# Kernel tuning notes

Measured on AMD Instinct MI355X. Metric: run time of the kernel, lower is better.

The kernel has to match this reference:

```python
import jax, jax.numpy as jnp
import numpy as np

V, B, S, DI, DH, DO = 32000, 32, 512, 256, 512, 128


def setup_inputs() -> dict:
    key = jax.random.key(0)
    ks = jax.random.split(key, 10)
    w = lambda k, shape: (jax.random.normal(k, shape, jnp.float32) * 0.02)
    z = lambda n: jnp.zeros((n,), jnp.float32)
    return {
        "tokens": jax.random.randint(ks[0], (B, S), 0, V, dtype=jnp.int32),
        "emb": w(ks[1], (V, DI)),
        "l0_Wz": w(ks[2], (DI + DH, DH)), "l0_bz": z(DH),
        "l0_Wr": w(ks[3], (DI + DH, DH)), "l0_br": z(DH),
        "l0_Wn": w(ks[4], (DI + DH, DH)), "l0_bn": z(DH),
        "l1_Wz": w(ks[5], (DH + DH, DH)), "l1_bz": z(DH),
        "l1_Wr": w(ks[6], (DH + DH, DH)), "l1_br": z(DH),
        "l1_Wn": w(ks[7], (DH + DH, DH)), "l1_bn": z(DH),
        "fc_W": w(ks[8], (DH, DO)), "fc_b": z(DO),
    }


def gru_layer(x_seq, Wz, bz, Wr, br, Wn, bn):
    # x_seq: [B, S, Din]; hidden dim inferred from Wz
    dh = Wz.shape[1]
    h0 = jnp.zeros((x_seq.shape[0], dh), x_seq.dtype)

    def step(H, x_t):
        comb = jnp.concatenate([x_t, H], axis=-1)          # [B, Din+DH]
        Z = jax.nn.sigmoid(comb @ Wz + bz)
        Rg = jax.nn.sigmoid(comb @ Wr + br)
        comb2 = jnp.concatenate([x_t, Rg * H], axis=-1)
        H_tilde = jnp.tanh(comb2 @ Wn + bn)
        Hn = (1.0 - Z) * H + Z * H_tilde
        return Hn, Hn

    _, ys = jax.lax.scan(step, h0, jnp.swapaxes(x_seq, 0, 1))  # [S, B, DH]
    return jnp.swapaxes(ys, 0, 1)                              # [B, S, DH]


def reference(tokens, emb,
              l0_Wz, l0_bz, l0_Wr, l0_br, l0_Wn, l0_bn,
              l1_Wz, l1_bz, l1_Wr, l1_br, l1_Wn, l1_bn,
              fc_W, fc_b):
    x = emb[tokens]                                            # [B, S, DI]
    x = gru_layer(x, l0_Wz, l0_bz, l0_Wr, l0_br, l0_Wn, l0_bn)
    x = gru_layer(x, l1_Wz, l1_bz, l1_Wr, l1_br, l1_Wn, l1_bn)
    logits = x @ fc_W + fc_b                                   # [B, S, DO]
    return jax.nn.log_softmax(logits, axis=-1)
```

## Files before the change

### kernel.cpp

```cpp
#include <hip/hip_runtime.h>
#include <hip/hip_bf16.h>
#include <cstdint>
#include <cstddef>


typedef short v8ss __attribute__((ext_vector_type(8)));
typedef float v4f  __attribute__((ext_vector_type(4)));
typedef unsigned short u16x8 __attribute__((ext_vector_type(8)));
typedef unsigned long long u64;

#define MFMA16(a, b, c) __builtin_amdgcn_mfma_f32_16x16x32_bf16((a), (b), (c), 0, 0, 0)

__device__ __forceinline__ unsigned short f2bf(float f) {
  union { float f; unsigned u; } v; v.f = f;
  unsigned r = v.u + 0x7fffu + ((v.u >> 16) & 1u);
  return (unsigned short)(r >> 16);
}
__device__ __forceinline__ unsigned short f2bfp(float f) {
  unsigned short h = f2bf(f);
  return (h == 0x8080u) ? (unsigned short)0x8081u : h;
}
__device__ __forceinline__ float bf2f(unsigned short h) {
  union { unsigned u; float f; } v; v.u = ((unsigned)h) << 16; return v.f;
}

#define S64   0x8080808080808080ull
#define INF64 0x7F807F807F807F80ull
#define POLL_LIM 16384

__device__ __forceinline__ u64 aload(const u64* p) {
  return __hip_atomic_load(p, __ATOMIC_RELAXED, __HIP_MEMORY_SCOPE_AGENT);
}
__device__ __forceinline__ void astore(u64* p, u64 v) {
  __hip_atomic_store(p, v, __ATOMIC_RELAXED, __HIP_MEMORY_SCOPE_AGENT);
}
__device__ __forceinline__ u64 spin8(const u64* p, int* dead) {
  u64 v = aload(p);
  if (v != S64) return v;
  int it = 0;
  for (;;) {
    __builtin_amdgcn_s_sleep(1);
    v = aload(p);
    if (v != S64) return v;
    if (*(volatile int*)dead) return v;
    if (++it > POLL_LIM) { *(volatile int*)dead = 1; return v; }
  }
}

#define BB   32
#define SS   512
#define DI   256
#define DH   512
#define DO   128
#define MROWS (BB * SS)
#define SLAB 16384

#define O_HX0   0
#define O_HX1   16809984
#define O_RHX0  33619968
#define O_RHX1  50397184
#define O_WT0X  67174400
#define O_WT0H  (O_WT0X + 1536*256*2)
#define O_WT1X  (O_WT0H + 16*96*512*2)
#define O_WT1H  (O_WT1X + 1536*512*2)
#define O_WTFC  (O_WT1H + 16*96*512*2)
#define O_XEMB  (O_WTFC + 128*512*2)

__global__ void prep_kernel(const float* __restrict__ l0Wz, const float* __restrict__ l0Wr,
                            const float* __restrict__ l0Wn,
                            const float* __restrict__ l1Wz, const float* __restrict__ l1Wr,
                            const float* __restrict__ l1Wn,
                            const float* __restrict__ fcW,
                            unsigned short* __restrict__ Wt0x, unsigned short* __restrict__ Wt0h,
                            unsigned short* __restrict__ Wt1x, unsigned short* __restrict__ Wt1h,
                            unsigned short* __restrict__ WtFC) {
  const int n0 = 1536 * 256;
  const int n1 = 16 * 96 * 512;
  const int n2 = 1536 * 512;
  const int n3 = 16 * 96 * 512;
  const int n4 = 128 * 512;
  const int total = n0 + n1 + n2 + n3 + n4;
  for (int i = blockIdx.x * 256 + threadIdx.x; i < total; i += gridDim.x * 256) {
    int j = i;
    if (j < n0) {
      int gcol = j / 256, k = j % 256, g = gcol >> 9, c = gcol & 511;
      const float* W = g == 0 ? l0Wz : (g == 1 ? l0Wr : l0Wn);
      Wt0x[j] = f2bf(W[k * 512 + c]); continue;
    }
    j -= n0;
    if (j < n1) {
      int r = j / (96 * 512), rem = j % (96 * 512), row = rem / 512, k = rem % 512;
      int g = row >> 5, c = r * 32 + (row & 31);
      const float* W = g == 0 ? l0Wz : (g == 1 ? l0Wr : l0Wn);
      Wt0h[j] = f2bf(W[(256 + k) * 512 + c]); continue;
    }
    j -= n1;
    if (j < n2) {
      int gcol = j / 512, k = j % 512, g = gcol >> 9, c = gcol & 511;
      const float* W = g == 0 ? l1Wz : (g == 1 ? l1Wr : l1Wn);
      Wt1x[j] = f2bf(W[k * 512 + c]); continue;
    }
    j -= n2;
    if (j < n3) {
      int r = j / (96 * 512), rem = j % (96 * 512), row = rem / 512, k = rem % 512;
      int g = row >> 5, c = r * 32 + (row & 31);
      const float* W = g == 0 ? l1Wz : (g == 1 ? l1Wr : l1Wn);
      Wt1h[j] = f2bf(W[(512 + k) * 512 + c]); continue;
    }
    j -= n3;
    { int c = j / 512, k = j % 512; WtFC[j] = f2bf(fcW[k * 128 + c]); }
  }
}

__global__ void embed_kernel(const int* __restrict__ tokens, const float* __restrict__ emb,
                             unsigned short* __restrict__ Xemb) {
  int r = blockIdx.x;
  int c = threadIdx.x;
  int t = r >> 5, b = r & 31;
  int tok = tokens[b * SS + t];
  Xemb[(size_t)r * DI + c] = f2bf(emb[(size_t)tok * DI + c]);
}

template <int LAYER>
__device__ __forceinline__ void gru_body(
    const int g, const int role, const int tid,
    const unsigned short* __restrict__ WtH,
    const unsigned short* __restrict__ Wx,
    const unsigned short* __restrict__ Xe,
    unsigned short* hx0,
    unsigned short* hx, unsigned short* rhx,
    const float* __restrict__ bz, const float* __restrict__ br,
    const float* __restrict__ bn,
    unsigned short* Wt, unsigned short* At, unsigned short* Rt, unsigned short* Xt,
    float* zbuf, float* hbuf, unsigned short* rstage, unsigned short* hstage,
    int* dead) {
  constexpr int K = LAYER ? 512 : 256;

  for (int ch = tid; ch < 96 * 64; ch += 256) {
    int row = ch >> 6, off = (ch & 63) * 8;
    *(u16x8*)&Wt[row * 520 + off] = *(const u16x8*)&WtH[((size_t)role * 96 + row) * 512 + off];
  }
  for (int i = tid * 8; i < 16 * 520; i += 256 * 8) {
    *(u16x8*)&At[i] = (u16x8)0;
    *(u16x8*)&Rt[i] = (u16x8)0;
    *(u16x8*)&Xt[i] = (u16x8)0;
  }
  if (tid < 128) { zbuf[tid] = 0.f; hbuf[tid] = 0.f; }
  __syncthreads();

  const int w = tid >> 6, l = tid & 63, cl = l & 15, kg = l >> 4;
  const int gate = w >> 1;
  const int lc16 = (w & 1) * 16;
  const int colA = role * 32 + lc16 + cl;
  const float biasA = (gate ? br : bz)[colA];
  const int lc16b = (w & 1) * 16;
  const int colB = role * 32 + lc16b + cl;
  const float biasB = (w < 2) ? bn[colB] : 0.f;

  const size_t gofs = (size_t)g * 2048;
  u64* atdst = (u64*)&At[(tid >> 6) * 520 + (tid & 63) * 8];
  u64* xtdst = (u64*)&Xt[(tid >> 6) * 520 + (tid & 63) * 8];
  const size_t pubofs = gofs + (size_t)(tid >> 3) * 512 + role * 32 + (tid & 7) * 4;
  const unsigned short* WxA = Wx + (size_t)(gate * 512 + colA) * K;
  const unsigned short* WxB = Wx + (size_t)(1024 + colB) * K;

  for (int t = 0; t < SS; ++t) {
    if (LAYER == 0) {
      if (tid < 128) {
        int j = tid >> 5, off = (tid & 31) * 8;
        *(u16x8*)&Xt[j * 520 + off] =
            *(const u16x8*)&Xe[((size_t)(t * 32) + 4 * g + j) * 256 + off];
      }
    } else {
      const u64* p = (const u64*)(hx0 + (size_t)(t + 1) * SLAB + gofs) + tid * 2;
      u64 lo = spin8(p, dead), hi = spin8(p + 1, dead);
      xtdst[0] = lo; xtdst[1] = hi;
    }
    {
      const u64* p = (const u64*)(hx + (size_t)t * SLAB + gofs) + tid * 2;
      u64 lo = spin8(p, dead), hi = spin8(p + 1, dead);
      atdst[0] = lo; atdst[1] = hi;
    }
    __syncthreads();
    if (*(volatile int*)dead) break;

    {
      v4f acc = {};
#pragma unroll
      for (int kc = 0; kc < K / 32; ++kc) {
        int ko = kc * 32 + kg * 8;
        v8ss a = *(const v8ss*)&Xt[cl * 520 + ko];
        v8ss b = *(const v8ss*)&WxA[ko];
        acc = MFMA16(a, b, acc);
      }
#pragma unroll
      for (int kc = 0; kc < 16; ++kc) {
        int ko = kc * 32 + kg * 8;
        v8ss a = *(const v8ss*)&At[cl * 520 + ko];
        v8ss b = *(const v8ss*)&Wt[(gate * 32 + lc16 + cl) * 520 + ko];
        acc = MFMA16(a, b, acc);
      }
      if (l < 16) {
        int lc = lc16 + cl;
#pragma unroll
        for (int j = 0; j < 4; ++j) {
          float pre = acc[j] + biasA;
          float gv = 1.f / (1.f + __expf(-pre));
          if (gate == 0) zbuf[j * 32 + lc] = gv;
          else           rstage[j * 32 + lc] = f2bfp(gv * hbuf[j * 32 + lc]);
        }
      }
    }
    __syncthreads();
    if (tid < 32)
      astore((u64*)(rhx + (size_t)t * SLAB + pubofs),
             *(const u64*)&rstage[(tid >> 3) * 32 + (tid & 7) * 4]);

    v4f accB = {};
    if (w >= 2) {
      int tt = tid & 127;
      int row = tt >> 5, c16 = (tt & 31) * 16;
      const u64* p = (const u64*)(rhx + (size_t)t * SLAB + gofs + (size_t)row * 512 + c16);
      u64* d = (u64*)&Rt[row * 520 + c16];
      d[0] = spin8(p, dead);     d[1] = spin8(p + 1, dead);
      d[2] = spin8(p + 2, dead); d[3] = spin8(p + 3, dead);
    } else {
#pragma unroll
      for (int kc = 0; kc < K / 32; ++kc) {
        int ko = kc * 32 + kg * 8;
        v8ss a = *(const v8ss*)&Xt[cl * 520 + ko];
        v8ss b = *(const v8ss*)&WxB[ko];
        accB = MFMA16(a, b, accB);
      }
    }
    __syncthreads();
    if (*(volatile int*)dead) break;

    if (w < 2) {
#pragma unroll
      for (int kc = 0; kc < 16; ++kc) {
        int ko = kc * 32 + kg * 8;
        v8ss a = *(const v8ss*)&Rt[cl * 520 + ko];
        v8ss b = *(const v8ss*)&Wt[(64 + lc16b + cl) * 520 + ko];
        accB = MFMA16(a, b, accB);
      }
      if (l < 16) {
        int lc = lc16b + cl;
#pragma unroll
        for (int j = 0; j < 4; ++j) {
          float pre = accB[j] + biasB;
          float ht = 1.f - 2.f / (__expf(2.f * pre) + 1.f);
          float z = zbuf[j * 32 + lc];
          float hn = (1.f - z) * hbuf[j * 32 + lc] + z * ht;
          hbuf[j * 32 + lc] = hn;
          hstage[j * 32 + lc] = f2bfp(hn);
        }
      }
    }
    __syncthreads();
    if (tid < 32)
      astore((u64*)(hx + (size_t)(t + 1) * SLAB + pubofs),
             *(const u64*)&hstage[(tid >> 3) * 32 + (tid & 7) * 4]);
  }

  if (*(volatile int*)dead) {
    for (int s = tid; s < SS * 8; s += 256) {
      int t2 = s >> 3, c8 = s & 7;
      size_t o = gofs + role * 32 + c8 * 4;
#pragma unroll
      for (int j = 0; j < 4; ++j) {
        astore((u64*)(hx + (size_t)(t2 + 1) * SLAB + o + (size_t)j * 512), INF64);
        astore((u64*)(rhx + (size_t)t2 * SLAB + o + (size_t)j * 512), INF64);
      }
    }
  }
}

__global__ __launch_bounds__(256, 1) void gru_fused(
    const unsigned short* __restrict__ Wt0h, const unsigned short* __restrict__ Wt1h,
    const unsigned short* __restrict__ Wt0x, const unsigned short* __restrict__ Wt1x,
    const unsigned short* __restrict__ Xemb,
    unsigned short* hx0, unsigned short* rhx0,
    unsigned short* hx1, unsigned short* rhx1,
    const float* bz0, const float* br0, const float* bn0,
    const float* bz1, const float* br1, const float* bn1) {
  __shared__ unsigned short Wt[96 * 520];
  __shared__ unsigned short At[16 * 520];
  __shared__ unsigned short Rt[16 * 520];
  __shared__ unsigned short Xt[16 * 520];
  __shared__ float zbuf[128], hbuf[128];
  __shared__ unsigned short rstage[128], hstage[128];
  __shared__ int dead;
  const int tid = threadIdx.x;
  if (tid == 0) dead = 0;
  const int layer = blockIdx.x >> 7, id = blockIdx.x & 127;
  const int g = id >> 4, role = id & 15;
  if (layer == 0)
    gru_body<0>(g, role, tid, Wt0h, Wt0x, Xemb, nullptr, hx0, rhx0, bz0, br0, bn0,
                Wt, At, Rt, Xt, zbuf, hbuf, rstage, hstage, &dead);
  else
    gru_body<1>(g, role, tid, Wt1h, Wt1x, nullptr, hx0, hx1, rhx1, bz1, br1, bn1,
                Wt, At, Rt, Xt, zbuf, hbuf, rstage, hstage, &dead);
}

__global__ __launch_bounds__(256) void fc_lsm_kernel(const unsigned short* __restrict__ Y1,
                                                     const unsigned short* __restrict__ WtFC,
                                                     const float* __restrict__ fcb,
                                                     float* __restrict__ out) {
  __shared__ float lout[32 * 128];
  int w = threadIdx.x >> 6, l = threadIdx.x & 63;
  int cl = l & 15, kg = l >> 4;
  int m0 = blockIdx.x * 32, n0 = w * 32;
  v4f acc[2][2] = {};
#pragma unroll
  for (int kc = 0; kc < 16; ++kc) {
    int ko = kc * 32 + kg * 8;
    v8ss a0 = *(const v8ss*)&Y1[(size_t)(m0 + cl) * 512 + ko];
    v8ss a1 = *(const v8ss*)&Y1[(size_t)(m0 + 16 + cl) * 512 + ko];
    v8ss b0 = *(const v8ss*)&WtFC[(size_t)(n0 + cl) * 512 + ko];
    v8ss b1 = *(const v8ss*)&WtFC[(size_t)(n0 + 16 + cl) * 512 + ko];
    acc[0][0] = MFMA16(a0, b0, acc[0][0]);
    acc[0][1] = MFMA16(a0, b1, acc[0][1]);
    acc[1][0] = MFMA16(a1, b0, acc[1][0]);
    acc[1][1] = MFMA16(a1, b1, acc[1][1]);
  }
#pragma unroll
  for (int mi = 0; mi < 2; ++mi)
#pragma unroll
    for (int ni = 0; ni < 2; ++ni) {
      int col = n0 + ni * 16 + cl;
      float bias = fcb[col];
#pragma unroll
      for (int r = 0; r < 4; ++r)
        lout[(mi * 16 + kg * 4 + r) * 128 + col] = acc[mi][ni][r] + bias;
    }
  __syncthreads();

  for (int rr = 0; rr < 8; ++rr) {
    int lr = w * 8 + rr;
    float a = lout[lr * 128 + l], b2 = lout[lr * 128 + 64 + l];
    float m = fmaxf(a, b2);
#pragma unroll
    for (int off = 32; off; off >>= 1) m = fmaxf(m, __shfl_xor(m, off));
    float s = __expf(a - m) + __expf(b2 - m);
#pragma unroll
    for (int off = 32; off; off >>= 1) s += __shfl_xor(s, off);
    float lse = m + logf(s);
    int mrow = m0 + lr, t = mrow >> 5, bb = mrow & 31;
    float* o = &out[((size_t)bb * SS + t) * 128];
    o[l] = a - lse;
    o[l + 64] = b2 - lse;
  }
}

extern "C" void kernel_launch(void* const* d_in, const int* in_sizes, int n_in,
                              void* d_out, int out_size, void* d_ws, size_t ws_size,
                              hipStream_t stream) {
  (void)in_sizes; (void)n_in; (void)out_size; (void)ws_size;
  const int*   tokens = (const int*)d_in[0];
  const float* emb    = (const float*)d_in[1];
  const float* l0Wz = (const float*)d_in[2];  const float* l0bz = (const float*)d_in[3];
  const float* l0Wr = (const float*)d_in[4];  const float* l0br = (const float*)d_in[5];
  const float* l0Wn = (const float*)d_in[6];  const float* l0bn = (const float*)d_in[7];
  const float* l1Wz = (const float*)d_in[8];  const float* l1bz = (const float*)d_in[9];
  const float* l1Wr = (const float*)d_in[10]; const float* l1br = (const float*)d_in[11];
  const float* l1Wn = (const float*)d_in[12]; const float* l1bn = (const float*)d_in[13];
  const float* fcW  = (const float*)d_in[14]; const float* fcb  = (const float*)d_in[15];

  char* ws = (char*)d_ws;
  unsigned short* hx0  = (unsigned short*)(ws + O_HX0);
  unsigned short* hx1  = (unsigned short*)(ws + O_HX1);
  unsigned short* rhx0 = (unsigned short*)(ws + O_RHX0);
  unsigned short* rhx1 = (unsigned short*)(ws + O_RHX1);
  unsigned short* Wt0x = (unsigned short*)(ws + O_WT0X);
  unsigned short* Wt0h = (unsigned short*)(ws + O_WT0H);
  unsigned short* Wt1x = (unsigned short*)(ws + O_WT1X);
  unsigned short* Wt1h = (unsigned short*)(ws + O_WT1H);
  unsigned short* WtFC = (unsigned short*)(ws + O_WTFC);
  unsigned short* Xemb = (unsigned short*)(ws + O_XEMB);

  hipMemsetAsync(hx0, 0x00, 32768, stream);
  hipMemsetAsync((char*)hx0 + 32768, 0x80, (size_t)SS * 32768, stream);
  hipMemsetAsync(hx1, 0x00, 32768, stream);
  hipMemsetAsync((char*)hx1 + 32768, 0x80, (size_t)SS * 32768, stream);
  hipMemsetAsync(rhx0, 0x80, (size_t)SS * 32768, stream);
  hipMemsetAsync(rhx1, 0x80, (size_t)SS * 32768, stream);

  prep_kernel<<<4096, 256, 0, stream>>>(l0Wz, l0Wr, l0Wn, l1Wz, l1Wr, l1Wn, fcW,
                                        Wt0x, Wt0h, Wt1x, Wt1h, WtFC);
  embed_kernel<<<MROWS, 256, 0, stream>>>(tokens, emb, Xemb);

  gru_fused<<<256, 256, 0, stream>>>(Wt0h, Wt1h, Wt0x, Wt1x, Xemb,
                                     hx0, rhx0, hx1, rhx1,
                                     l0bz, l0br, l0bn, l1bz, l1br, l1bn);

  fc_lsm_kernel<<<512, 256, 0, stream>>>(hx1 + SLAB, WtFC, fcb, (float*)d_out);
}
```

Before: 3.250 ms.

## Publish GRU gate outputs directly per element and poll with batched sentinel checks

The r*h and new-h values are now written to the global exchange buffers straight from the computing lanes as 16-bit atomic stores. This replaces staging them in shared memory, adding a __syncthreads, and publishing 64-bit chunks. Because those chunks can now arrive partially written, the spin-wait loops load several 64-bit words at once and test every 16-bit lane against the sentinel. In layer 1 the x and h waits are merged into one loop, and in layer 0 the embedding load is issued before the wait. The aim is to remove a block-wide barrier from each half-step and shorten the critical path of the cross-block recurrence, at the cost of many more small global stores.

```diff
diff --git a/kernel.cpp b/kernel.cpp
--- a/kernel.cpp
+++ b/kernel.cpp
@@ -34,17 +34,44 @@
 __device__ __forceinline__ void astore(u64* p, u64 v) {
   __hip_atomic_store(p, v, __ATOMIC_RELAXED, __HIP_MEMORY_SCOPE_AGENT);
 }
-__device__ __forceinline__ u64 spin8(const u64* p, int* dead) {
-  u64 v = aload(p);
-  if (v != S64) return v;
+__device__ __forceinline__ void astore16(unsigned short* p, unsigned short v) {
+  __hip_atomic_store(p, v, __ATOMIC_RELAXED, __HIP_MEMORY_SCOPE_AGENT);
+}
+__device__ __forceinline__ int hz16(u64 x) {
+  return ((x - 0x0001000100010001ull) & ~x & 0x8000800080008000ull) != 0ull;
+}
+__device__ __forceinline__ void spin2(const u64* p, u64* o, int* dead) {
+  u64 a = aload(p), b = aload(p + 1);
   int it = 0;
-  for (;;) {
+  while (hz16(a ^ S64) | hz16(b ^ S64)) {
+    if (*(volatile int*)dead) break;
+    if (++it > POLL_LIM) { *(volatile int*)dead = 1; break; }
     __builtin_amdgcn_s_sleep(1);
-    v = aload(p);
-    if (v != S64) return v;
-    if (*(volatile int*)dead) return v;
-    if (++it > POLL_LIM) { *(volatile int*)dead = 1; return v; }
-  }
+    a = aload(p); b = aload(p + 1);
+  }
+  o[0] = a; o[1] = b;
+}
+__device__ __forceinline__ void spin4(const u64* p, u64* o, int* dead) {
+  u64 a = aload(p), b = aload(p + 1), c = aload(p + 2), d = aload(p + 3);
+  int it = 0;
+  while (hz16(a ^ S64) | hz16(b ^ S64) | hz16(c ^ S64) | hz16(d ^ S64)) {
+    if (*(volatile int*)dead) break;
+    if (++it > POLL_LIM) { *(volatile int*)dead = 1; break; }
+    __builtin_amdgcn_s_sleep(1);
+    a = aload(p); b = aload(p + 1); c = aload(p + 2); d = aload(p + 3);
+  }
+  o[0] = a; o[1] = b; o[2] = c; o[3] = d;
+}
+__device__ __forceinline__ void spin22(const u64* p, const u64* q, u64* o, int* dead) {
+  u64 a = aload(p), b = aload(p + 1), c = aload(q), d = aload(q + 1);
+  int it = 0;
+  while (hz16(a ^ S64) | hz16(b ^ S64) | hz16(c ^ S64) | hz16(d ^ S64)) {
+    if (*(volatile int*)dead) break;
+    if (++it > POLL_LIM) { *(volatile int*)dead = 1; break; }
+    __builtin_amdgcn_s_sleep(1);
+    a = aload(p); b = aload(p + 1); c = aload(q); d = aload(q + 1);
+  }
+  o[0] = a; o[1] = b; o[2] = c; o[3] = d;
 }
 
 #define BB   32
@@ -132,8 +159,7 @@
     const float* __restrict__ bz, const float* __restrict__ br,
     const float* __restrict__ bn,
     unsigned short* Wt, unsigned short* At, unsigned short* Rt, unsigned short* Xt,
-    float* zbuf, float* hbuf, unsigned short* rstage, unsigned short* hstage,
-    int* dead) {
+    float* zbuf, float* hbuf, int* dead) {
   constexpr int K = LAYER ? 512 : 256;
 
   for (int ch = tid; ch < 96 * 64; ch += 256) {
@@ -160,26 +186,32 @@
   const size_t gofs = (size_t)g * 2048;
   u64* atdst = (u64*)&At[(tid >> 6) * 520 + (tid & 63) * 8];
   u64* xtdst = (u64*)&Xt[(tid >> 6) * 520 + (tid & 63) * 8];
-  const size_t pubofs = gofs + (size_t)(tid >> 3) * 512 + role * 32 + (tid & 7) * 4;
+  const int tt = tid & 127;
+  const int prow = tt >> 5, pc16 = (tt & 31) * 16;
+  u64* rtdst = (u64*)&Rt[prow * 520 + pc16];
   const unsigned short* WxA = Wx + (size_t)(gate * 512 + colA) * K;
   const unsigned short* WxB = Wx + (size_t)(1024 + colB) * K;
 
   for (int t = 0; t < SS; ++t) {
     if (LAYER == 0) {
+      u16x8 xreg;
       if (tid < 128) {
         int j = tid >> 5, off = (tid & 31) * 8;
-        *(u16x8*)&Xt[j * 520 + off] =
-            *(const u16x8*)&Xe[((size_t)(t * 32) + 4 * g + j) * 256 + off];
+        xreg = *(const u16x8*)&Xe[((size_t)(t * 32) + 4 * g + j) * 256 + off];
+      }
+      u64 o[2];
+      spin2((const u64*)(hx + (size_t)t * SLAB + gofs) + tid * 2, o, dead);
+      atdst[0] = o[0]; atdst[1] = o[1];
+      if (tid < 128) {
+        int j = tid >> 5, off = (tid & 31) * 8;
+        *(u16x8*)&Xt[j * 520 + off] = xreg;
       }
     } else {
-      const u64* p = (const u64*)(hx0 + (size_t)(t + 1) * SLAB + gofs) + tid * 2;
-      u64 lo = spin8(p, dead), hi = spin8(p + 1, dead);
-      xtdst[0] = lo; xtdst[1] = hi;
-    }
-    {
-      const u64* p = (const u64*)(hx + (size_t)t * SLAB + gofs) + tid * 2;
-      u64 lo = spin8(p, dead), hi = spin8(p + 1, dead);
-      atdst[0] = lo; atdst[1] = hi;
+      u64 o[4];
+      spin22((const u64*)(hx0 + (size_t)(t + 1) * SLAB + gofs) + tid * 2,
+             (const u64*)(hx + (size_t)t * SLAB + gofs) + tid * 2, o, dead);
+      xtdst[0] = o[0]; xtdst[1] = o[1];
+      atdst[0] = o[2]; atdst[1] = o[3];
     }
     __syncthreads();
     if (*(volatile int*)dead) break;
@@ -206,24 +238,20 @@
         for (int j = 0; j < 4; ++j) {
           float pre = acc[j] + biasA;
           float gv = 1.f / (1.f + __expf(-pre));
-          if (gate == 0) zbuf[j * 32 + lc] = gv;
-          else           rstage[j * 32 + lc] = f2bfp(gv * hbuf[j * 32 + lc]);
+          if (gate == 0) {
+            zbuf[j * 32 + lc] = gv;
+          } else {
+            astore16(&rhx[(size_t)t * SLAB + gofs + (size_t)j * 512 + colA],
+                     f2bfp(gv * hbuf[j * 32 + lc]));
+          }
         }
       }
     }
-    __syncthreads();
-    if (tid < 32)
-      astore((u64*)(rhx + (size_t)t * SLAB + pubofs),
-             *(const u64*)&rstage[(tid >> 3) * 32 + (tid & 7) * 4]);
-
     v4f accB = {};
     if (w >= 2) {
-      int tt = tid & 127;
-      int row = tt >> 5, c16 = (tt & 31) * 16;
-      const u64* p = (const u64*)(rhx + (size_t)t * SLAB + gofs + (size_t)row * 512 + c16);
-      u64* d = (u64*)&Rt[row * 520 + c16];
-      d[0] = spin8(p, dead);     d[1] = spin8(p + 1, dead);
-      d[2] = spin8(p + 2, dead); d[3] = spin8(p + 3, dead);
+      u64 o[4];
+      spin4((const u64*)(rhx + (size_t)t * SLAB + gofs + (size_t)prow * 512 + pc16), o, dead);
+      rtdst[0] = o[0]; rtdst[1] = o[1]; rtdst[2] = o[2]; rtdst[3] = o[3];
     } else {
 #pragma unroll
       for (int kc = 0; kc < K / 32; ++kc) {
@@ -253,14 +281,12 @@
           float z = zbuf[j * 32 + lc];
           float hn = (1.f - z) * hbuf[j * 32 + lc] + z * ht;
           hbuf[j * 32 + lc] = hn;
-          hstage[j * 32 + lc] = f2bfp(hn);
+          astore16(&hx[(size_t)(t + 1) * SLAB + gofs + (size_t)j * 512 + colB],
+                   f2bfp(hn));
         }
       }
     }
     __syncthreads();
-    if (tid < 32)
-      astore((u64*)(hx + (size_t)(t + 1) * SLAB + pubofs),
-             *(const u64*)&hstage[(tid >> 3) * 32 + (tid & 7) * 4]);
   }
 
   if (*(volatile int*)dead) {
@@ -289,7 +315,6 @@
   __shared__ unsigned short Rt[16 * 520];
   __shared__ unsigned short Xt[16 * 520];
   __shared__ float zbuf[128], hbuf[128];
-  __shared__ unsigned short rstage[128], hstage[128];
   __shared__ int dead;
   const int tid = threadIdx.x;
   if (tid == 0) dead = 0;
@@ -297,10 +322,10 @@
   const int g = id >> 4, role = id & 15;
   if (layer == 0)
     gru_body<0>(g, role, tid, Wt0h, Wt0x, Xemb, nullptr, hx0, rhx0, bz0, br0, bn0,
-                Wt, At, Rt, Xt, zbuf, hbuf, rstage, hstage, &dead);
+                Wt, At, Rt, Xt, zbuf, hbuf, &dead);
   else
     gru_body<1>(g, role, tid, Wt1h, Wt1x, nullptr, hx0, hx1, rhx1, bz1, br1, bn1,
-                Wt, At, Rt, Xt, zbuf, hbuf, rstage, hstage, &dead);
+                Wt, At, Rt, Xt, zbuf, hbuf, &dead);
 }
 
 __global__ __launch_bounds__(256) void fc_lsm_kernel(const unsigned short* __restrict__ Y1,
```

Result: slower. 3.480 ms (+7.1%).
